# Kernel tuning notes

Hardware: AMD Instinct MI355X
Metric: run time of the kernel (lower is better)

## Reference

```python
import jax, jax.numpy as jnp
import numpy as np

N_NODES = 50000
N_EDGES = 800000
E_DIM = 128
N_LAYERS = 3
IN_DIM = 2
OUT_DIM = 1


def _lin_init(key, fan_in, fan_out, scale=None):
    # rough kaiming-tanh init, exact values don't matter for correctness testing
    s = scale if scale is not None else (5.0 / 3.0) / np.sqrt(fan_in)
    return jax.random.normal(key, (fan_in, fan_out), dtype=jnp.float32) * s


def setup_inputs() -> dict:
    key = jax.random.key(0)
    ks = jax.random.split(key, 16)
    node_feature = jax.random.normal(ks[0], (N_NODES, IN_DIM), dtype=jnp.float32)
    edge_index = jax.random.randint(ks[1], (2, N_EDGES), 0, N_NODES)
    batch = jnp.zeros((N_NODES,), dtype=jnp.int32)

    enc_W = _lin_init(ks[2], IN_DIM, E_DIM)
    enc_b = jnp.zeros((E_DIM,), dtype=jnp.float32)

    def stack(k, fan_in, fan_out):
        kk = jax.random.split(k, N_LAYERS)
        return jnp.stack([_lin_init(kk[i], fan_in, fan_out) for i in range(N_LAYERS)])

    gate_W = stack(ks[3], E_DIM, E_DIM)
    gate_b = jnp.zeros((N_LAYERS, E_DIM), dtype=jnp.float32)
    att_W = stack(ks[4], E_DIM, E_DIM)
    att_b = jnp.zeros((N_LAYERS, E_DIM), dtype=jnp.float32)
    msg_W = stack(ks[5], E_DIM, E_DIM)
    msg_b = jnp.zeros((N_LAYERS, E_DIM), dtype=jnp.float32)
    upd_W = stack(ks[6], 2 * E_DIM, E_DIM)
    upd_b = jnp.zeros((N_LAYERS, E_DIM), dtype=jnp.float32)

    dec1_W = _lin_init(ks[7], E_DIM, E_DIM // 2)
    dec1_b = jnp.zeros((E_DIM // 2,), dtype=jnp.float32)
    dec2_W = _lin_init(ks[8], E_DIM // 2, OUT_DIM, scale=1.0 / np.sqrt(E_DIM // 2))
    dec2_b = jnp.zeros((OUT_DIM,), dtype=jnp.float32)

    return dict(node_feature=node_feature, edge_index=edge_index, batch=batch,
                enc_W=enc_W, enc_b=enc_b,
                gate_W=gate_W, gate_b=gate_b, att_W=att_W, att_b=att_b,
                msg_W=msg_W, msg_b=msg_b, upd_W=upd_W, upd_b=upd_b,
                dec1_W=dec1_W, dec1_b=dec1_b, dec2_W=dec2_W, dec2_b=dec2_b)


def _segment_softmax(x, seg, num_segments):
    # PyG softmax over segments, numerically stable, per-channel
    m = jax.ops.segment_max(x, seg, num_segments=num_segments)
    m = jnp.where(jnp.isfinite(m), m, 0.0)
    e = jnp.exp(x - m[seg])
    s = jax.ops.segment_sum(e, seg, num_segments=num_segments)
    return e / (s[seg] + 1e-16)


def reference(node_feature, edge_index, batch,
              enc_W, enc_b, gate_W, gate_b, att_W, att_b,
              msg_W, msg_b, upd_W, upd_b,
              dec1_W, dec1_b, dec2_W, dec2_b):
    n = node_feature.shape[0]
    src, dst = edge_index[0], edge_index[1]  # j -> i (source_to_target)
    h = jnp.tanh(node_feature @ enc_W + enc_b)  # [N, E_DIM]
    for l in range(N_LAYERS):
        mj = jnp.tanh(h[src] @ msg_W[l] + msg_b[l])          # messages [Edges, E_DIM]
        gate = mj @ gate_W[l] + gate_b[l]                     # gate_nn (Linear only)
        alpha = _segment_softmax(gate, dst, n)                # softmax over incoming edges
        v = jnp.tanh(mj @ att_W[l] + att_b[l])                # attention_mlp
        aggr = jax.ops.segment_sum(alpha * v, dst, num_segments=n)
        h = jnp.tanh(jnp.concatenate([h, aggr], axis=1) @ upd_W[l] + upd_b[l])
    out = jnp.tanh(h @ dec1_W + dec1_b)
    out = out @ dec2_W + dec2_b
    return out
```

## Files before the change

### kernel.cpp

```cpp
#include <hip/hip_runtime.h>
#include <math.h>

#define ED 128
#define PROW 256

typedef _Float16 f16;
typedef _Float16 half8 __attribute__((ext_vector_type(8)));
typedef _Float16 half4 __attribute__((ext_vector_type(4)));
typedef float f32x4 __attribute__((ext_vector_type(4)));

static __device__ __forceinline__ float tanh_fast(float x) {
  float ax = fabsf(x);
  float e = __expf(2.0f * ax);
  float t = 1.0f - 2.0f / (e + 1.0f);
  return __builtin_copysignf(t, x);
}

template <int NT, int NBYTES>
static __device__ __forceinline__ void stage256(
    const char* __restrict__ gsrc, char* lds, int tid) {
  #pragma unroll
  for (int i = 0; i < NBYTES / (NT * 16); ++i) {
    int b = (i * NT + tid) * 16;
    int row = b >> 8;
    int sw = (b & 255) ^ ((row & 7) << 4);
    float4 v = *reinterpret_cast<const float4*>(gsrc + (size_t)row * 256 + sw);
    *reinterpret_cast<float4*>(lds + b) = v;
  }
}

static __device__ __forceinline__ half8 read_w(const char* Wsb, int col, int koff) {
  int byte = col * 256 + (koff ^ ((col & 7) << 4));
  return *reinterpret_cast<const half8*>(Wsb + byte);
}

template <int NT>
static __device__ __forceinline__ void stage512(
    const char* __restrict__ gsrc, char* lds, int tid) {
  #pragma unroll
  for (int i = 0; i < 32768 / (NT * 16); ++i) {
    int b = (i * NT + tid) * 16;
    int row = b >> 9;
    int sw = (b & 511) ^ ((row & 7) << 4);
    float4 v = *reinterpret_cast<const float4*>(gsrc + (size_t)row * 512 + sw);
    *reinterpret_cast<float4*>(lds + b) = v;
  }
}

static __device__ __forceinline__ half8 read_w512(const char* Wsb, int colL, int koff) {
  int byte = colL * 512 + (koff ^ ((colL & 7) << 4));
  return *reinterpret_cast<const half8*>(Wsb + byte);
}

__global__ __launch_bounds__(256) void encoder_kernel(
    const float* __restrict__ x, const float* __restrict__ W,
    const float* __restrict__ b, f16* __restrict__ h, int n) {
  int idx = blockIdx.x * blockDim.x + threadIdx.x;
  if (idx >= n * ED) return;
  int i = idx >> 7, c = idx & 127;
  float v = x[i * 2 + 0] * W[c] + x[i * 2 + 1] * W[ED + c] + b[c];
  h[idx] = (f16)tanh_fast(v);
}

__global__ __launch_bounds__(256) void transpose_w_kernel(
    const float* __restrict__ src, f16* __restrict__ dst, int K, int C, int total) {
  int idx = blockIdx.x * 256 + threadIdx.x;
  if (idx >= total) return;
  int kc = K * C;
  int m = idx / kc;
  int rem = idx - m * kc;
  int c = rem / K;
  int k = rem - c * K;
  dst[idx] = (f16)src[(size_t)m * kc + (size_t)k * C + c];
}

__global__ __launch_bounds__(256) void transpose3_kernel(
    const float* __restrict__ s0, const float* __restrict__ s1,
    const float* __restrict__ s2, f16* __restrict__ d0,
    f16* __restrict__ d1, f16* __restrict__ d2) {
  int idx = blockIdx.x * 256 + threadIdx.x;
  const int per = 3 * 128 * 128;
  int which = idx / per;
  if (which >= 3) return;
  int rem = idx - which * per;
  const float* s = (which == 0) ? s0 : (which == 1) ? s1 : s2;
  f16* d = (which == 0) ? d0 : (which == 1) ? d1 : d2;
  int m = rem >> 14;
  int r2 = rem & 16383;
  int c = r2 >> 7, k = r2 & 127;
  d[rem] = (f16)s[m * 16384 + k * 128 + c];
}

__global__ __launch_bounds__(256) void count_deg_kernel(
    const int* __restrict__ dst, int* __restrict__ deg, int E) {
  int e = blockIdx.x * blockDim.x + threadIdx.x;
  if (e < E) atomicAdd(&deg[dst[e]], 1);
}

__global__ __launch_bounds__(1024) void scan_kernel(
    const int* __restrict__ deg, int* __restrict__ offs,
    int* __restrict__ cursor, int n) {
  __shared__ int wsum[16];
  __shared__ int carry_s;
  const int tid = threadIdx.x;
  const int lane = tid & 63;
  const int wid = tid >> 6;
  if (tid == 0) carry_s = 0;
  __syncthreads();
  for (int base = 0; base < n; base += 1024) {
    const int i = base + tid;
    const int v = (i < n) ? deg[i] : 0;
    int x = v;
    #pragma unroll
    for (int d = 1; d < 64; d <<= 1) {
      int t = __shfl_up(x, d, 64);
      if (lane >= d) x += t;
    }
    if (lane == 63) wsum[wid] = x;
    __syncthreads();
    int wbase = 0, total = 0;
    #pragma unroll
    for (int w = 0; w < 16; ++w) {
      int s = wsum[w];
      if (w < wid) wbase += s;
      total += s;
    }
    const int carry = carry_s;
    if (i < n) {
      const int excl = carry + wbase + x - v;
      offs[i] = excl;
      cursor[i] = excl;
    }
    __syncthreads();
    if (tid == 0) carry_s = carry + total;
    __syncthreads();
  }
  if (tid == 0) offs[n] = carry_s;
}

__global__ __launch_bounds__(256) void scatter_kernel(
    const int* __restrict__ src, const int* __restrict__ dst,
    int* __restrict__ cursor, int* __restrict__ ssrc, int E) {
  int e = blockIdx.x * blockDim.x + threadIdx.x;
  if (e < E) {
    int d = dst[e];
    int pos = atomicAdd(&cursor[d], 1);
    ssrc[pos] = src[e];
  }
}


__global__ __launch_bounds__(512, 4) void gemm_mgv_kernel(
    const f16* __restrict__ h,
    const f16* __restrict__ mWt, const float* __restrict__ mb,
    const f16* __restrict__ gWt, const float* __restrict__ gb,
    const f16* __restrict__ aWt, const float* __restrict__ ab,
    f16* __restrict__ P, int n) {
  __shared__ f16 Ws[128 * 128];
  __shared__ f16 Ss[128 * 128];
  char* Wsb = reinterpret_cast<char*>(Ws);
  char* Sb = reinterpret_cast<char*>(Ss);
  const int tid = threadIdx.x;
  const int w = tid >> 6, lane = tid & 63;
  const int lr = lane & 15, lg = lane >> 4;
  const int r0 = blockIdx.x * 128 + w * 16;

  half8 a[4];
  {
    int rr = r0 + lr;
    if (rr >= n) rr = n - 1;
    const f16* ap = h + (size_t)rr * ED + lg * 8;
    #pragma unroll
    for (int kt = 0; kt < 4; ++kt)
      a[kt] = *reinterpret_cast<const half8*>(ap + kt * 32);
  }

  stage256<512, 32768>((const char*)mWt, Wsb, tid);
  __syncthreads();
  #pragma unroll
  for (int t = 0; t < 8; ++t) {
    f32x4 acc = {0.f, 0.f, 0.f, 0.f};
    int col = t * 16 + lr;
    #pragma unroll
    for (int kt = 0; kt < 4; ++kt)
      acc = __builtin_amdgcn_mfma_f32_16x16x32_f16(a[kt], read_w(Wsb, col, lg * 16 + kt * 64), acc, 0, 0, 0);
    float bias = mb[col];
    #pragma unroll
    for (int j = 0; j < 4; ++j) {
      int srow = w * 16 + lg * 4 + j;
      int byte = srow * 256 + (((col * 2) ^ ((srow & 7) << 4)));
      *reinterpret_cast<f16*>(Sb + byte) = (f16)tanh_fast(acc[j] + bias);
    }
  }
  half8 ma[4];
  {
    int lrow = w * 16 + lr;
    #pragma unroll
    for (int kt = 0; kt < 4; ++kt) {
      int byte = lrow * 256 + ((lg * 16 + kt * 64) ^ ((lrow & 7) << 4));
      ma[kt] = *reinterpret_cast<const half8*>(Sb + byte);
    }
  }
  __syncthreads();

  stage256<512, 32768>((const char*)gWt, Wsb, tid);
  __syncthreads();
  #pragma unroll
  for (int t = 0; t < 8; ++t) {
    f32x4 acc = {0.f, 0.f, 0.f, 0.f};
    int col = t * 16 + lr;
    #pragma unroll
    for (int kt = 0; kt < 4; ++kt)
      acc = __builtin_amdgcn_mfma_f32_16x16x32_f16(ma[kt], read_w(Wsb, col, lg * 16 + kt * 64), acc, 0, 0, 0);
    float bias = gb[col];
    #pragma unroll
    for (int j = 0; j < 4; ++j) {
      int grow = r0 + lg * 4 + j;
      if (grow < n)
        P[(size_t)grow * PROW + col] = (f16)fminf(__expf(acc[j] + bias), 60000.f);
    }
  }
  __syncthreads();

  stage256<512, 32768>((const char*)aWt, Wsb, tid);
  __syncthreads();
  #pragma unroll
  for (int t = 0; t < 8; ++t) {
    f32x4 acc = {0.f, 0.f, 0.f, 0.f};
    int col = t * 16 + lr;
    #pragma unroll
    for (int kt = 0; kt < 4; ++kt)
      acc = __builtin_amdgcn_mfma_f32_16x16x32_f16(ma[kt], read_w(Wsb, col, lg * 16 + kt * 64), acc, 0, 0, 0);
    float bias = ab[col];
    #pragma unroll
    for (int j = 0; j < 4; ++j) {
      int grow = r0 + lg * 4 + j;
      if (grow < n) {
        float wld = (float)P[(size_t)grow * PROW + col];
        P[(size_t)grow * PROW + 128 + col] = (f16)(wld * tanh_fast(acc[j] + bias));
      }
    }
  }
}

__global__ __launch_bounds__(512, 4) void updmgv_kernel(
    const f16* __restrict__ h, const f16* __restrict__ ag,
    const f16* __restrict__ uWt, const float* __restrict__ ub,
    const f16* __restrict__ mWt, const float* __restrict__ mb,
    const f16* __restrict__ gWt, const float* __restrict__ gb,
    const f16* __restrict__ aWt, const float* __restrict__ ab,
    f16* __restrict__ hout, f16* __restrict__ P, int n) {
  __shared__ f16 Ws[128 * 128];
  __shared__ f16 Ss[128 * 128];
  char* Wsb = reinterpret_cast<char*>(Ws);
  char* Sb = reinterpret_cast<char*>(Ss);
  const int tid = threadIdx.x;
  const int w = tid >> 6, lane = tid & 63;
  const int lr = lane & 15, lg = lane >> 4;
  const int r0 = blockIdx.x * 128 + w * 16;

  half8 ah[4], aa[4];
  {
    int rr = r0 + lr;
    if (rr >= n) rr = n - 1;
    const f16* ap = h + (size_t)rr * ED + lg * 8;
    const f16* bp = ag + (size_t)rr * ED + lg * 8;
    #pragma unroll
    for (int kt = 0; kt < 4; ++kt) {
      ah[kt] = *reinterpret_cast<const half8*>(ap + kt * 32);
      aa[kt] = *reinterpret_cast<const half8*>(bp + kt * 32);
    }
  }

  #pragma unroll
  for (int half = 0; half < 2; ++half) {
    __syncthreads();
    stage512<512>((const char*)uWt + (size_t)half * 64 * 512, Wsb, tid);
    __syncthreads();
    #pragma unroll
    for (int t = 0; t < 4; ++t) {
      int colL = t * 16 + lr;
      int col = half * 64 + colL;
      f32x4 acc = {0.f, 0.f, 0.f, 0.f};
      #pragma unroll
      for (int kt = 0; kt < 4; ++kt)
        acc = __builtin_amdgcn_mfma_f32_16x16x32_f16(ah[kt], read_w512(Wsb, colL, lg * 16 + kt * 64), acc, 0, 0, 0);
      #pragma unroll
      for (int kt = 0; kt < 4; ++kt)
        acc = __builtin_amdgcn_mfma_f32_16x16x32_f16(aa[kt], read_w512(Wsb, colL, 256 + lg * 16 + kt * 64), acc, 0, 0, 0);
      float bias = ub[col];
      #pragma unroll
      for (int j = 0; j < 4; ++j) {
        f16 hv = (f16)tanh_fast(acc[j] + bias);
        int srow = w * 16 + lg * 4 + j;
        int byte = srow * 256 + (((col * 2) ^ ((srow & 7) << 4)));
        *reinterpret_cast<f16*>(Sb + byte) = hv;
        int grow = r0 + lg * 4 + j;
        if (grow < n) hout[(size_t)grow * ED + col] = hv;
      }
    }
  }
  half8 ha[4];
  {
    int lrow = w * 16 + lr;
    #pragma unroll
    for (int kt = 0; kt < 4; ++kt) {
      int byte = lrow * 256 + ((lg * 16 + kt * 64) ^ ((lrow & 7) << 4));
      ha[kt] = *reinterpret_cast<const half8*>(Sb + byte);
    }
  }
  __syncthreads();

  stage256<512, 32768>((const char*)mWt, Wsb, tid);
  __syncthreads();
  #pragma unroll
  for (int t = 0; t < 8; ++t) {
    f32x4 acc = {0.f, 0.f, 0.f, 0.f};
    int col = t * 16 + lr;
    #pragma unroll
    for (int kt = 0; kt < 4; ++kt)
      acc = __builtin_amdgcn_mfma_f32_16x16x32_f16(ha[kt], read_w(Wsb, col, lg * 16 + kt * 64), acc, 0, 0, 0);
    float bias = mb[col];
    #pragma unroll
    for (int j = 0; j < 4; ++j) {
      int srow = w * 16 + lg * 4 + j;
      int byte = srow * 256 + (((col * 2) ^ ((srow & 7) << 4)));
      *reinterpret_cast<f16*>(Sb + byte) = (f16)tanh_fast(acc[j] + bias);
    }
  }
  half8 ma[4];
  {
    int lrow = w * 16 + lr;
    #pragma unroll
    for (int kt = 0; kt < 4; ++kt) {
      int byte = lrow * 256 + ((lg * 16 + kt * 64) ^ ((lrow & 7) << 4));
      ma[kt] = *reinterpret_cast<const half8*>(Sb + byte);
    }
  }
  __syncthreads();

  stage256<512, 32768>((const char*)gWt, Wsb, tid);
  __syncthreads();
  #pragma unroll
  for (int t = 0; t < 8; ++t) {
    f32x4 acc = {0.f, 0.f, 0.f, 0.f};
    int col = t * 16 + lr;
    #pragma unroll
    for (int kt = 0; kt < 4; ++kt)
      acc = __builtin_amdgcn_mfma_f32_16x16x32_f16(ma[kt], read_w(Wsb, col, lg * 16 + kt * 64), acc, 0, 0, 0);
    float bias = gb[col];
    #pragma unroll
    for (int j = 0; j < 4; ++j) {
      int grow = r0 + lg * 4 + j;
      if (grow < n)
        P[(size_t)grow * PROW + col] = (f16)fminf(__expf(acc[j] + bias), 60000.f);
    }
  }
  __syncthreads();

  stage256<512, 32768>((const char*)aWt, Wsb, tid);
  __syncthreads();
  #pragma unroll
  for (int t = 0; t < 8; ++t) {
    f32x4 acc = {0.f, 0.f, 0.f, 0.f};
    int col = t * 16 + lr;
    #pragma unroll
    for (int kt = 0; kt < 4; ++kt)
      acc = __builtin_amdgcn_mfma_f32_16x16x32_f16(ma[kt], read_w(Wsb, col, lg * 16 + kt * 64), acc, 0, 0, 0);
    float bias = ab[col];
    #pragma unroll
    for (int j = 0; j < 4; ++j) {
      int grow = r0 + lg * 4 + j;
      if (grow < n) {
        float wld = (float)P[(size_t)grow * PROW + col];
        P[(size_t)grow * PROW + 128 + col] = (f16)(wld * tanh_fast(acc[j] + bias));
      }
    }
  }
}

__global__ __launch_bounds__(512, 4) void upddec_kernel(
    const f16* __restrict__ h, const f16* __restrict__ ag,
    const f16* __restrict__ uWt, const float* __restrict__ ub,
    const f16* __restrict__ d1Wt, const float* __restrict__ d1b,
    const float* __restrict__ d2W, const float* __restrict__ d2b,
    float* __restrict__ out, int n) {
  __shared__ f16 Ws[128 * 128];
  __shared__ f16 Ss[128 * 128];
  char* Wsb = reinterpret_cast<char*>(Ws);
  char* Sb = reinterpret_cast<char*>(Ss);
  const int tid = threadIdx.x;
  const int w = tid >> 6, lane = tid & 63;
  const int lr = lane & 15, lg = lane >> 4;
  const int r0 = blockIdx.x * 128 + w * 16;

  half8 ah[4], aa[4];
  {
    int rr = r0 + lr;
    if (rr >= n) rr = n - 1;
    const f16* ap = h + (size_t)rr * ED + lg * 8;
    const f16* bp = ag + (size_t)rr * ED + lg * 8;
    #pragma unroll
    for (int kt = 0; kt < 4; ++kt) {
      ah[kt] = *reinterpret_cast<const half8*>(ap + kt * 32);
      aa[kt] = *reinterpret_cast<const half8*>(bp + kt * 32);
    }
  }

  #pragma unroll
  for (int half = 0; half < 2; ++half) {
    __syncthreads();
    stage512<512>((const char*)uWt + (size_t)half * 64 * 512, Wsb, tid);
    __syncthreads();
    #pragma unroll
    for (int t = 0; t < 4; ++t) {
      int colL = t * 16 + lr;
      int col = half * 64 + colL;
      f32x4 acc = {0.f, 0.f, 0.f, 0.f};
      #pragma unroll
      for (int kt = 0; kt < 4; ++kt)
        acc = __builtin_amdgcn_mfma_f32_16x16x32_f16(ah[kt], read_w512(Wsb, colL, lg * 16 + kt * 64), acc, 0, 0, 0);
      #pragma unroll
      for (int kt = 0; kt < 4; ++kt)
        acc = __builtin_amdgcn_mfma_f32_16x16x32_f16(aa[kt], read_w512(Wsb, colL, 256 + lg * 16 + kt * 64), acc, 0, 0, 0);
      float bias = ub[col];
      #pragma unroll
      for (int j = 0; j < 4; ++j) {
        int srow = w * 16 + lg * 4 + j;
        int byte = srow * 256 + (((col * 2) ^ ((srow & 7) << 4)));
        *reinterpret_cast<f16*>(Sb + byte) = (f16)tanh_fast(acc[j] + bias);
      }
    }
  }
  half8 ha[4];
  {
    int lrow = w * 16 + lr;
    #pragma unroll
    for (int kt = 0; kt < 4; ++kt) {
      int byte = lrow * 256 + ((lg * 16 + kt * 64) ^ ((lrow & 7) << 4));
      ha[kt] = *reinterpret_cast<const half8*>(Sb + byte);
    }
  }
  __syncthreads();

  stage256<512, 16384>((const char*)d1Wt, Wsb, tid);
  __syncthreads();
  float rowsum[4] = {0.f, 0.f, 0.f, 0.f};
  #pragma unroll
  for (int t = 0; t < 4; ++t) {
    f32x4 acc = {0.f, 0.f, 0.f, 0.f};
    int col = t * 16 + lr;
    #pragma unroll
    for (int kt = 0; kt < 4; ++kt)
      acc = __builtin_amdgcn_mfma_f32_16x16x32_f16(ha[kt], read_w(Wsb, col, lg * 16 + kt * 64), acc, 0, 0, 0);
    float b1 = d1b[col], w2 = d2W[col];
    #pragma unroll
    for (int j = 0; j < 4; ++j) rowsum[j] += tanh_fast(acc[j] + b1) * w2;
  }
  #pragma unroll
  for (int d = 1; d < 16; d <<= 1) {
    #pragma unroll
    for (int j = 0; j < 4; ++j) rowsum[j] += __shfl_xor(rowsum[j], d, 64);
  }
  if (lr == 0) {
    #pragma unroll
    for (int j = 0; j < 4; ++j) {
      int grow = r0 + lg * 4 + j;
      if (grow < n) out[grow] = rowsum[j] + d2b[0];
    }
  }
}

__global__ __launch_bounds__(256) void edge_aggr_kernel(
    const int* __restrict__ offs, const int* __restrict__ ssrc,
    const f16* __restrict__ P, f16* __restrict__ aggr, int n) {
  int i = blockIdx.x * 4 + (threadIdx.x >> 6);
  if (i >= n) return;
  int lane = threadIdx.x & 63;
  int s0 = offs[i], s1 = offs[i + 1];
  const char* Pb = reinterpret_cast<const char*>(P);

  float4 acc = {0.f, 0.f, 0.f, 0.f};
  #pragma unroll 4
  for (int e = s0; e < s1; ++e) {
    int sn = ssrc[e];
    half4 x = *reinterpret_cast<const half4*>(Pb + (size_t)sn * 512 + lane * 8);
    acc.x += (float)x.x;
    acc.y += (float)x.y;
    acc.z += (float)x.z;
    acc.w += (float)x.w;
  }
  float px = __shfl(acc.x, lane ^ 32, 64);
  float py = __shfl(acc.y, lane ^ 32, 64);
  float pz = __shfl(acc.z, lane ^ 32, 64);
  float pw = __shfl(acc.w, lane ^ 32, 64);
  if (lane >= 32) {
    half4 o;
    o.x = (f16)(acc.x / (px + 1e-16f));
    o.y = (f16)(acc.y / (py + 1e-16f));
    o.z = (f16)(acc.z / (pz + 1e-16f));
    o.w = (f16)(acc.w / (pw + 1e-16f));
    *reinterpret_cast<half4*>(
        reinterpret_cast<char*>(aggr) + (size_t)i * 256 + (size_t)(lane - 32) * 8) = o;
  }
}

extern "C" void kernel_launch(void* const* d_in, const int* in_sizes, int n_in,
                              void* d_out, int out_size, void* d_ws, size_t ws_size,
                              hipStream_t stream) {
  const float* node_feature = (const float*)d_in[0];
  const int*   edge_index   = (const int*)d_in[1];
  const float* enc_W  = (const float*)d_in[3];
  const float* enc_b  = (const float*)d_in[4];
  const float* gate_W = (const float*)d_in[5];
  const float* gate_b = (const float*)d_in[6];
  const float* att_W  = (const float*)d_in[7];
  const float* att_b  = (const float*)d_in[8];
  const float* msg_W  = (const float*)d_in[9];
  const float* msg_b  = (const float*)d_in[10];
  const float* upd_W  = (const float*)d_in[11];
  const float* upd_b  = (const float*)d_in[12];
  const float* dec1_W = (const float*)d_in[13];
  const float* dec1_b = (const float*)d_in[14];
  const float* dec2_W = (const float*)d_in[15];
  const float* dec2_b = (const float*)d_in[16];

  const int n = in_sizes[0] / 2;
  const int E = in_sizes[1] / 2;
  const int* src = edge_index;
  const int* dst = edge_index + E;

  char* ws = (char*)d_ws;
  size_t off = 0;
  auto alloc = [&](size_t bytes) -> void* {
    void* p = ws + off;
    off += (bytes + 255) & ~(size_t)255;
    return p;
  };
  f16* hA   = (f16*)alloc((size_t)n * ED * 2);
  f16* hB   = (f16*)alloc((size_t)n * ED * 2);
  f16* P    = (f16*)alloc((size_t)n * PROW * 2);
  f16* aggr = (f16*)alloc((size_t)n * ED * 2);
  int* deg    = (int*)alloc((size_t)n * 4);
  int* offs   = (int*)alloc((size_t)(n + 1) * 4);
  int* cursor = (int*)alloc((size_t)n * 4);
  int* ssrc   = (int*)alloc((size_t)E * 4);
  f16* msgT  = (f16*)alloc((size_t)3 * ED * ED * 2);
  f16* gateT = (f16*)alloc((size_t)3 * ED * ED * 2);
  f16* attT  = (f16*)alloc((size_t)3 * ED * ED * 2);
  f16* updT  = (f16*)alloc((size_t)3 * ED * 2 * ED * 2);
  f16* dec1T = (f16*)alloc((size_t)ED * 64 * 2);

  {
    int tot3 = 3 * 3 * ED * ED;
    transpose3_kernel<<<(tot3 + 255) / 256, 256, 0, stream>>>(
        msg_W, gate_W, att_W, msgT, gateT, attT);
    int totu = 3 * 2 * ED * ED;
    transpose_w_kernel<<<(totu + 255) / 256, 256, 0, stream>>>(
        upd_W, updT, 2 * ED, ED, totu);
    int totd = ED * 64;
    transpose_w_kernel<<<(totd + 255) / 256, 256, 0, stream>>>(
        dec1_W, dec1T, ED, 64, totd);
  }

  hipMemsetAsync(deg, 0, (size_t)n * 4, stream);
  count_deg_kernel<<<(E + 255) / 256, 256, 0, stream>>>(dst, deg, E);
  scan_kernel<<<1, 1024, 0, stream>>>(deg, offs, cursor, n);
  scatter_kernel<<<(E + 255) / 256, 256, 0, stream>>>(src, dst, cursor, ssrc, E);

  encoder_kernel<<<((size_t)n * ED + 255) / 256, 256, 0, stream>>>(
      node_feature, enc_W, enc_b, hA, n);

  const int gemm_grid = (n + 127) / 128;
  const int aggr_grid = (n + 3) / 4;

  gemm_mgv_kernel<<<gemm_grid, 512, 0, stream>>>(
      hA, msgT, msg_b, gateT, gate_b, attT, att_b, P, n);
  edge_aggr_kernel<<<aggr_grid, 256, 0, stream>>>(offs, ssrc, P, aggr, n);

  updmgv_kernel<<<gemm_grid, 512, 0, stream>>>(
      hA, aggr, updT, upd_b,
      msgT + (size_t)1 * ED * ED, msg_b + ED,
      gateT + (size_t)1 * ED * ED, gate_b + ED,
      attT + (size_t)1 * ED * ED, att_b + ED,
      hB, P, n);
  edge_aggr_kernel<<<aggr_grid, 256, 0, stream>>>(offs, ssrc, P, aggr, n);

  updmgv_kernel<<<gemm_grid, 512, 0, stream>>>(
      hB, aggr, updT + (size_t)1 * 2 * ED * ED, upd_b + ED,
      msgT + (size_t)2 * ED * ED, msg_b + 2 * ED,
      gateT + (size_t)2 * ED * ED, gate_b + 2 * ED,
      attT + (size_t)2 * ED * ED, att_b + 2 * ED,
      hA, P, n);
  edge_aggr_kernel<<<aggr_grid, 256, 0, stream>>>(offs, ssrc, P, aggr, n);

  upddec_kernel<<<gemm_grid, 512, 0, stream>>>(
      hA, aggr, updT + (size_t)2 * 2 * ED * ED, upd_b + 2 * ED,
      dec1T, dec1_b, dec2_W, dec2_b, (float*)d_out, n);
}
```

Baseline: 447.9 us.

## Prefetch weight panels into registers and interleave P layout to drop readback

Weight staging into LDS is split into a register load and an LDS write, so the next panel's global load is issued before the current GEMM and its latency overlaps compute. The gate and attention GEMMs are reordered: attention tanh values are held in registers, then the gate exp is computed and both (weight, weight*value) are written as interleaved half2 pairs. This removes the global read-back of P and the cross-lane shuffle and divide split in edge aggregation. The cost is extra register pressure from the prefetched panels and the tq array, which under the launch bounds could cause spills.

```diff
diff --git a/kernel.cpp b/kernel.cpp
--- a/kernel.cpp
+++ b/kernel.cpp
@@ -7,6 +7,7 @@
 typedef _Float16 f16;
 typedef _Float16 half8 __attribute__((ext_vector_type(8)));
 typedef _Float16 half4 __attribute__((ext_vector_type(4)));
+typedef _Float16 half2v __attribute__((ext_vector_type(2)));
 typedef float f32x4 __attribute__((ext_vector_type(4)));
 
 static __device__ __forceinline__ float tanh_fast(float x) {
@@ -16,37 +17,35 @@
   return __builtin_copysignf(t, x);
 }
 
-template <int NT, int NBYTES>
-static __device__ __forceinline__ void stage256(
-    const char* __restrict__ gsrc, char* lds, int tid) {
-  #pragma unroll
-  for (int i = 0; i < NBYTES / (NT * 16); ++i) {
+template <int NI>
+struct Panel { float4 v[NI]; };
+
+template <int NI, int NT, int RB>
+static __device__ __forceinline__ Panel<NI> panel_load(
+    const char* __restrict__ g, int tid) {
+  Panel<NI> p;
+  #pragma unroll
+  for (int i = 0; i < NI; ++i) {
     int b = (i * NT + tid) * 16;
-    int row = b >> 8;
-    int sw = (b & 255) ^ ((row & 7) << 4);
-    float4 v = *reinterpret_cast<const float4*>(gsrc + (size_t)row * 256 + sw);
-    *reinterpret_cast<float4*>(lds + b) = v;
-  }
+    int row = b / RB;
+    int sw = (b % RB) ^ ((row & 7) << 4);
+    p.v[i] = *reinterpret_cast<const float4*>(g + (size_t)row * RB + sw);
+  }
+  return p;
+}
+
+template <int NI, int NT>
+static __device__ __forceinline__ void panel_write(
+    char* lds, const Panel<NI>& p, int tid) {
+  #pragma unroll
+  for (int i = 0; i < NI; ++i)
+    *reinterpret_cast<float4*>(lds + (size_t)(i * NT + tid) * 16) = p.v[i];
 }
 
 static __device__ __forceinline__ half8 read_w(const char* Wsb, int col, int koff) {
   int byte = col * 256 + (koff ^ ((col & 7) << 4));
   return *reinterpret_cast<const half8*>(Wsb + byte);
 }
-
-template <int NT>
-static __device__ __forceinline__ void stage512(
-    const char* __restrict__ gsrc, char* lds, int tid) {
-  #pragma unroll
-  for (int i = 0; i < 32768 / (NT * 16); ++i) {
-    int b = (i * NT + tid) * 16;
-    int row = b >> 9;
-    int sw = (b & 511) ^ ((row & 7) << 4);
-    float4 v = *reinterpret_cast<const float4*>(gsrc + (size_t)row * 512 + sw);
-    *reinterpret_cast<float4*>(lds + b) = v;
-  }
-}
-
 static __device__ __forceinline__ half8 read_w512(const char* Wsb, int colL, int koff) {
   int byte = colL * 512 + (koff ^ ((colL & 7) << 4));
   return *reinterpret_cast<const half8*>(Wsb + byte);
@@ -161,10 +160,11 @@
   char* Wsb = reinterpret_cast<char*>(Ws);
   char* Sb = reinterpret_cast<char*>(Ss);
   const int tid = threadIdx.x;
-  const int w = tid >> 6, lane = tid & 63;
+  const int wd = tid >> 6, lane = tid & 63;
   const int lr = lane & 15, lg = lane >> 4;
-  const int r0 = blockIdx.x * 128 + w * 16;
-
+  const int r0 = blockIdx.x * 128 + wd * 16;
+
+  Panel<4> nx = panel_load<4, 512, 256>((const char*)mWt, tid);
   half8 a[4];
   {
     int rr = r0 + lr;
@@ -174,9 +174,10 @@
     for (int kt = 0; kt < 4; ++kt)
       a[kt] = *reinterpret_cast<const half8*>(ap + kt * 32);
   }
-
-  stage256<512, 32768>((const char*)mWt, Wsb, tid);
-  __syncthreads();
+  panel_write<4, 512>(Wsb, nx, tid);
+  nx = panel_load<4, 512, 256>((const char*)aWt, tid);
+  __syncthreads();
+
   #pragma unroll
   for (int t = 0; t < 8; ++t) {
     f32x4 acc = {0.f, 0.f, 0.f, 0.f};
@@ -187,14 +188,14 @@
     float bias = mb[col];
     #pragma unroll
     for (int j = 0; j < 4; ++j) {
-      int srow = w * 16 + lg * 4 + j;
+      int srow = wd * 16 + lg * 4 + j;
       int byte = srow * 256 + (((col * 2) ^ ((srow & 7) << 4)));
       *reinterpret_cast<f16*>(Sb + byte) = (f16)tanh_fast(acc[j] + bias);
     }
   }
   half8 ma[4];
   {
-    int lrow = w * 16 + lr;
+    int lrow = wd * 16 + lr;
     #pragma unroll
     for (int kt = 0; kt < 4; ++kt) {
       int byte = lrow * 256 + ((lg * 16 + kt * 64) ^ ((lrow & 7) << 4));
@@ -202,9 +203,26 @@
     }
   }
   __syncthreads();
-
-  stage256<512, 32768>((const char*)gWt, Wsb, tid);
-  __syncthreads();
+  panel_write<4, 512>(Wsb, nx, tid);
+  nx = panel_load<4, 512, 256>((const char*)gWt, tid);
+  __syncthreads();
+
+  half4 tq[8];
+  #pragma unroll
+  for (int t = 0; t < 8; ++t) {
+    f32x4 acc = {0.f, 0.f, 0.f, 0.f};
+    int col = t * 16 + lr;
+    #pragma unroll
+    for (int kt = 0; kt < 4; ++kt)
+      acc = __builtin_amdgcn_mfma_f32_16x16x32_f16(ma[kt], read_w(Wsb, col, lg * 16 + kt * 64), acc, 0, 0, 0);
+    float bias = ab[col];
+    #pragma unroll
+    for (int j = 0; j < 4; ++j) tq[t][j] = (f16)tanh_fast(acc[j] + bias);
+  }
+  __syncthreads();
+  panel_write<4, 512>(Wsb, nx, tid);
+  __syncthreads();
+
   #pragma unroll
   for (int t = 0; t < 8; ++t) {
     f32x4 acc = {0.f, 0.f, 0.f, 0.f};
@@ -216,28 +234,12 @@
     #pragma unroll
     for (int j = 0; j < 4; ++j) {
       int grow = r0 + lg * 4 + j;
-      if (grow < n)
-        P[(size_t)grow * PROW + col] = (f16)fminf(__expf(acc[j] + bias), 60000.f);
-    }
-  }
-  __syncthreads();
-
-  stage256<512, 32768>((const char*)aWt, Wsb, tid);
-  __syncthreads();
-  #pragma unroll
-  for (int t = 0; t < 8; ++t) {
-    f32x4 acc = {0.f, 0.f, 0.f, 0.f};
-    int col = t * 16 + lr;
-    #pragma unroll
-    for (int kt = 0; kt < 4; ++kt)
-      acc = __builtin_amdgcn_mfma_f32_16x16x32_f16(ma[kt], read_w(Wsb, col, lg * 16 + kt * 64), acc, 0, 0, 0);
-    float bias = ab[col];
-    #pragma unroll
-    for (int j = 0; j < 4; ++j) {
-      int grow = r0 + lg * 4 + j;
       if (grow < n) {
-        float wld = (float)P[(size_t)grow * PROW + col];
-        P[(size_t)grow * PROW + 128 + col] = (f16)(wld * tanh_fast(acc[j] + bias));
+        float wexp = fminf(__expf(acc[j] + bias), 60000.f);
+        half2v pr;
+        pr.x = (f16)wexp;
+        pr.y = (f16)(wexp * (float)tq[t][j]);
+        *reinterpret_cast<half2v*>(P + (size_t)grow * PROW + col * 2) = pr;
       }
     }
   }
@@ -255,10 +257,11 @@
   char* Wsb = reinterpret_cast<char*>(Ws);
   char* Sb = reinterpret_cast<char*>(Ss);
   const int tid = threadIdx.x;
-  const int w = tid >> 6, lane = tid & 63;
+  const int wd = tid >> 6, lane = tid & 63;
   const int lr = lane & 15, lg = lane >> 4;
-  const int r0 = blockIdx.x * 128 + w * 16;
-
+  const int r0 = blockIdx.x * 128 + wd * 16;
+
+  Panel<4> nx = panel_load<4, 512, 512>((const char*)uWt, tid);
   half8 ah[4], aa[4];
   {
     int rr = r0 + lr;
@@ -271,38 +274,62 @@
       aa[kt] = *reinterpret_cast<const half8*>(bp + kt * 32);
     }
   }
-
-  #pragma unroll
-  for (int half = 0; half < 2; ++half) {
-    __syncthreads();
-    stage512<512>((const char*)uWt + (size_t)half * 64 * 512, Wsb, tid);
-    __syncthreads();
-    #pragma unroll
-    for (int t = 0; t < 4; ++t) {
-      int colL = t * 16 + lr;
-      int col = half * 64 + colL;
-      f32x4 acc = {0.f, 0.f, 0.f, 0.f};
-      #pragma unroll
-      for (int kt = 0; kt < 4; ++kt)
-        acc = __builtin_amdgcn_mfma_f32_16x16x32_f16(ah[kt], read_w512(Wsb, colL, lg * 16 + kt * 64), acc, 0, 0, 0);
-      #pragma unroll
-      for (int kt = 0; kt < 4; ++kt)
-        acc = __builtin_amdgcn_mfma_f32_16x16x32_f16(aa[kt], read_w512(Wsb, colL, 256 + lg * 16 + kt * 64), acc, 0, 0, 0);
-      float bias = ub[col];
-      #pragma unroll
-      for (int j = 0; j < 4; ++j) {
-        f16 hv = (f16)tanh_fast(acc[j] + bias);
-        int srow = w * 16 + lg * 4 + j;
-        int byte = srow * 256 + (((col * 2) ^ ((srow & 7) << 4)));
-        *reinterpret_cast<f16*>(Sb + byte) = hv;
-        int grow = r0 + lg * 4 + j;
-        if (grow < n) hout[(size_t)grow * ED + col] = hv;
-      }
+  panel_write<4, 512>(Wsb, nx, tid);
+  nx = panel_load<4, 512, 512>((const char*)uWt + 64 * 512, tid);
+  __syncthreads();
+
+  #pragma unroll
+  for (int t = 0; t < 4; ++t) {
+    int colL = t * 16 + lr;
+    int col = colL;
+    f32x4 acc = {0.f, 0.f, 0.f, 0.f};
+    #pragma unroll
+    for (int kt = 0; kt < 4; ++kt)
+      acc = __builtin_amdgcn_mfma_f32_16x16x32_f16(ah[kt], read_w512(Wsb, colL, lg * 16 + kt * 64), acc, 0, 0, 0);
+    #pragma unroll
+    for (int kt = 0; kt < 4; ++kt)
+      acc = __builtin_amdgcn_mfma_f32_16x16x32_f16(aa[kt], read_w512(Wsb, colL, 256 + lg * 16 + kt * 64), acc, 0, 0, 0);
+    float bias = ub[col];
+    #pragma unroll
+    for (int j = 0; j < 4; ++j) {
+      f16 hv = (f16)tanh_fast(acc[j] + bias);
+      int srow = wd * 16 + lg * 4 + j;
+      int byte = srow * 256 + (((col * 2) ^ ((srow & 7) << 4)));
+      *reinterpret_cast<f16*>(Sb + byte) = hv;
+      int grow = r0 + lg * 4 + j;
+      if (grow < n) hout[(size_t)grow * ED + col] = hv;
+    }
+  }
+  __syncthreads();
+  panel_write<4, 512>(Wsb, nx, tid);
+  nx = panel_load<4, 512, 256>((const char*)mWt, tid);
+  __syncthreads();
+
+  #pragma unroll
+  for (int t = 0; t < 4; ++t) {
+    int colL = t * 16 + lr;
+    int col = 64 + colL;
+    f32x4 acc = {0.f, 0.f, 0.f, 0.f};
+    #pragma unroll
+    for (int kt = 0; kt < 4; ++kt)
+      acc = __builtin_amdgcn_mfma_f32_16x16x32_f16(ah[kt], read_w512(Wsb, colL, lg * 16 + kt * 64), acc, 0, 0, 0);
+    #pragma unroll
+    for (int kt = 0; kt < 4; ++kt)
+      acc = __builtin_amdgcn_mfma_f32_16x16x32_f16(aa[kt], read_w512(Wsb, colL, 256 + lg * 16 + kt * 64), acc, 0, 0, 0);
+    float bias = ub[col];
+    #pragma unroll
+    for (int j = 0; j < 4; ++j) {
+      f16 hv = (f16)tanh_fast(acc[j] + bias);
+      int srow = wd * 16 + lg * 4 + j;
+      int byte = srow * 256 + (((col * 2) ^ ((srow & 7) << 4)));
+      *reinterpret_cast<f16*>(Sb + byte) = hv;
+      int grow = r0 + lg * 4 + j;
+      if (grow < n) hout[(size_t)grow * ED + col] = hv;
     }
   }
   half8 ha[4];
   {
-    int lrow = w * 16 + lr;
+    int lrow = wd * 16 + lr;
     #pragma unroll
     for (int kt = 0; kt < 4; ++kt) {
       int byte = lrow * 256 + ((lg * 16 + kt * 64) ^ ((lrow & 7) << 4));
@@ -310,9 +337,10 @@
     }
   }
   __syncthreads();
-
-  stage256<512, 32768>((const char*)mWt, Wsb, tid);
-  __syncthreads();
+  panel_write<4, 512>(Wsb, nx, tid);
+  nx = panel_load<4, 512, 256>((const char*)aWt, tid);
+  __syncthreads();
+
   #pragma unroll
   for (int t = 0; t < 8; ++t) {
     f32x4 acc = {0.f, 0.f, 0.f, 0.f};
@@ -323,14 +351,14 @@
     float bias = mb[col];
     #pragma unroll
     for (int j = 0; j < 4; ++j) {
-      int srow = w * 16 + lg * 4 + j;
+      int srow = wd * 16 + lg * 4 + j;
       int byte = srow * 256 + (((col * 2) ^ ((srow & 7) << 4)));
       *reinterpret_cast<f16*>(Sb + byte) = (f16)tanh_fast(acc[j] + bias);
     }
   }
   half8 ma[4];
   {
-    int lrow = w * 16 + lr;
+    int lrow = wd * 16 + lr;
     #pragma unroll
     for (int kt = 0; kt < 4; ++kt) {
       int byte = lrow * 256 + ((lg * 16 + kt * 64) ^ ((lrow & 7) << 4));
@@ -338,9 +366,26 @@
     }
   }
   __syncthreads();
-
-  stage256<512, 32768>((const char*)gWt, Wsb, tid);
-  __syncthreads();
+  panel_write<4, 512>(Wsb, nx, tid);
+  nx = panel_load<4, 512, 256>((const char*)gWt, tid);
+  __syncthreads();
+
+  half4 tq[8];
+  #pragma unroll
+  for (int t = 0; t < 8; ++t) {
+    f32x4 acc = {0.f, 0.f, 0.f, 0.f};
+    int col = t * 16 + lr;
+    #pragma unroll
+    for (int kt = 0; kt < 4; ++kt)
+      acc = __builtin_amdgcn_mfma_f32_16x16x32_f16(ma[kt], read_w(Wsb, col, lg * 16 + kt * 64), acc, 0, 0, 0);
+    float bias = ab[col];
+    #pragma unroll
+    for (int j = 0; j < 4; ++j) tq[t][j] = (f16)tanh_fast(acc[j] + bias);
+  }
+  __syncthreads();
+  panel_write<4, 512>(Wsb, nx, tid);
+  __syncthreads();
+
   #pragma unroll
   for (int t = 0; t < 8; ++t) {
     f32x4 acc = {0.f, 0.f, 0.f, 0.f};
@@ -352,28 +397,12 @@
     #pragma unroll
     for (int j = 0; j < 4; ++j) {
       int grow = r0 + lg * 4 + j;
-      if (grow < n)
-        P[(size_t)grow * PROW + col] = (f16)fminf(__expf(acc[j] + bias), 60000.f);
-    }
-  }
-  __syncthreads();
-
-  stage256<512, 32768>((const char*)aWt, Wsb, tid);
-  __syncthreads();
-  #pragma unroll
-  for (int t = 0; t < 8; ++t) {
-    f32x4 acc = {0.f, 0.f, 0.f, 0.f};
-    int col = t * 16 + lr;
-    #pragma unroll
-    for (int kt = 0; kt < 4; ++kt)
-      acc = __builtin_amdgcn_mfma_f32_16x16x32_f16(ma[kt], read_w(Wsb, col, lg * 16 + kt * 64), acc, 0, 0, 0);
-    float bias = ab[col];
-    #pragma unroll
-    for (int j = 0; j < 4; ++j) {
-      int grow = r0 + lg * 4 + j;
       if (grow < n) {
-        float wld = (float)P[(size_t)grow * PROW + col];
-        P[(size_t)grow * PROW + 128 + col] = (f16)(wld * tanh_fast(acc[j] + bias));
+        float wexp = fminf(__expf(acc[j] + bias), 60000.f);
+        half2v pr;
+        pr.x = (f16)wexp;
+        pr.y = (f16)(wexp * (float)tq[t][j]);
+        *reinterpret_cast<half2v*>(P + (size_t)grow * PROW + col * 2) = pr;
       }
     }
   }
@@ -390,10 +419,11 @@
   char* Wsb = reinterpret_cast<char*>(Ws);
   char* Sb = reinterpret_cast<char*>(Ss);
   const int tid = threadIdx.x;
-  const int w = tid >> 6, lane = tid & 63;
+  const int wd = tid >> 6, lane = tid & 63;
   const int lr = lane & 15, lg = lane >> 4;
-  const int r0 = blockIdx.x * 128 + w * 16;
-
+  const int r0 = blockIdx.x * 128 + wd * 16;
+
+  Panel<4> nx = panel_load<4, 512, 512>((const char*)uWt, tid);
   half8 ah[4], aa[4];
   {
     int rr = r0 + lr;
@@ -406,35 +436,56 @@
       aa[kt] = *reinterpret_cast<const half8*>(bp + kt * 32);
     }
   }
-
-  #pragma unroll
-  for (int half = 0; half < 2; ++half) {
-    __syncthreads();
-    stage512<512>((const char*)uWt + (size_t)half * 64 * 512, Wsb, tid);
-    __syncthreads();
-    #pragma unroll
-    for (int t = 0; t < 4; ++t) {
-      int colL = t * 16 + lr;
-      int col = half * 64 + colL;
-      f32x4 acc = {0.f, 0.f, 0.f, 0.f};
-      #pragma unroll
-      for (int kt = 0; kt < 4; ++kt)
-        acc = __builtin_amdgcn_mfma_f32_16x16x32_f16(ah[kt], read_w512(Wsb, colL, lg * 16 + kt * 64), acc, 0, 0, 0);
-      #pragma unroll
-      for (int kt = 0; kt < 4; ++kt)
-        acc = __builtin_amdgcn_mfma_f32_16x16x32_f16(aa[kt], read_w512(Wsb, colL, 256 + lg * 16 + kt * 64), acc, 0, 0, 0);
-      float bias = ub[col];
-      #pragma unroll
-      for (int j = 0; j < 4; ++j) {
-        int srow = w * 16 + lg * 4 + j;
-        int byte = srow * 256 + (((col * 2) ^ ((srow & 7) << 4)));
-        *reinterpret_cast<f16*>(Sb + byte) = (f16)tanh_fast(acc[j] + bias);
-      }
+  panel_write<4, 512>(Wsb, nx, tid);
+  nx = panel_load<4, 512, 512>((const char*)uWt + 64 * 512, tid);
+  __syncthreads();
+
+  #pragma unroll
+  for (int t = 0; t < 4; ++t) {
+    int colL = t * 16 + lr;
+    int col = colL;
+    f32x4 acc = {0.f, 0.f, 0.f, 0.f};
+    #pragma unroll
+    for (int kt = 0; kt < 4; ++kt)
+      acc = __builtin_amdgcn_mfma_f32_16x16x32_f16(ah[kt], read_w512(Wsb, colL, lg * 16 + kt * 64), acc, 0, 0, 0);
+    #pragma unroll
+    for (int kt = 0; kt < 4; ++kt)
+      acc = __builtin_amdgcn_mfma_f32_16x16x32_f16(aa[kt], read_w512(Wsb, colL, 256 + lg * 16 + kt * 64), acc, 0, 0, 0);
+    float bias = ub[col];
+    #pragma unroll
+    for (int j = 0; j < 4; ++j) {
+      int srow = wd * 16 + lg * 4 + j;
+      int byte = srow * 256 + (((col * 2) ^ ((srow & 7) << 4)));
+      *reinterpret_cast<f16*>(Sb + byte) = (f16)tanh_fast(acc[j] + bias);
+    }
+  }
+  __syncthreads();
+  panel_write<4, 512>(Wsb, nx, tid);
+  Panel<2> nd = panel_load<2, 512, 256>((const char*)d1Wt, tid);
+  __syncthreads();
+
+  #pragma unroll
+  for (int t = 0; t < 4; ++t) {
+    int colL = t * 16 + lr;
+    int col = 64 + colL;
+    f32x4 acc = {0.f, 0.f, 0.f, 0.f};
+    #pragma unroll
+    for (int kt = 0; kt < 4; ++kt)
+      acc = __builtin_amdgcn_mfma_f32_16x16x32_f16(ah[kt], read_w512(Wsb, colL, lg * 16 + kt * 64), acc, 0, 0, 0);
+    #pragma unroll
+    for (int kt = 0; kt < 4; ++kt)
+      acc = __builtin_amdgcn_mfma_f32_16x16x32_f16(aa[kt], read_w512(Wsb, colL, 256 + lg * 16 + kt * 64), acc, 0, 0, 0);
+    float bias = ub[col];
+    #pragma unroll
+    for (int j = 0; j < 4; ++j) {
+      int srow = wd * 16 + lg * 4 + j;
+      int byte = srow * 256 + (((col * 2) ^ ((srow & 7) << 4)));
+      *reinterpret_cast<f16*>(Sb + byte) = (f16)tanh_fast(acc[j] + bias);
     }
   }
   half8 ha[4];
   {
-    int lrow = w * 16 + lr;
+    int lrow = wd * 16 + lr;
     #pragma unroll
     for (int kt = 0; kt < 4; ++kt) {
       int byte = lrow * 256 + ((lg * 16 + kt * 64) ^ ((lrow & 7) << 4));
@@ -442,9 +493,9 @@
     }
   }
   __syncthreads();
-
-  stage256<512, 16384>((const char*)d1Wt, Wsb, tid);
-  __syncthreads();
+  panel_write<2, 512>(Wsb, nd, tid);
+  __syncthreads();
+
   float rowsum[4] = {0.f, 0.f, 0.f, 0.f};
   #pragma unroll
   for (int t = 0; t < 4; ++t) {
@@ -480,29 +531,21 @@
   int s0 = offs[i], s1 = offs[i + 1];
   const char* Pb = reinterpret_cast<const char*>(P);
 
-  float4 acc = {0.f, 0.f, 0.f, 0.f};
+  float sw0 = 0.f, wv0 = 0.f, sw1 = 0.f, wv1 = 0.f;
   #pragma unroll 4
   for (int e = s0; e < s1; ++e) {
     int sn = ssrc[e];
     half4 x = *reinterpret_cast<const half4*>(Pb + (size_t)sn * 512 + lane * 8);
-    acc.x += (float)x.x;
-    acc.y += (float)x.y;
-    acc.z += (float)x.z;
-    acc.w += (float)x.w;
-  }
-  float px = __shfl(acc.x, lane ^ 32, 64);
-  float py = __shfl(acc.y, lane ^ 32, 64);
-  float pz = __shfl(acc.z, lane ^ 32, 64);
-  float pw = __shfl(acc.w, lane ^ 32, 64);
-  if (lane >= 32) {
-    half4 o;
-    o.x = (f16)(acc.x / (px + 1e-16f));
-    o.y = (f16)(acc.y / (py + 1e-16f));
-    o.z = (f16)(acc.z / (pz + 1e-16f));
-    o.w = (f16)(acc.w / (pw + 1e-16f));
-    *reinterpret_cast<half4*>(
-        reinterpret_cast<char*>(aggr) + (size_t)i * 256 + (size_t)(lane - 32) * 8) = o;
-  }
+    sw0 += (float)x.x;
+    wv0 += (float)x.y;
+    sw1 += (float)x.z;
+    wv1 += (float)x.w;
+  }
+  half2v o;
+  o.x = (f16)(wv0 / (sw0 + 1e-16f));
+  o.y = (f16)(wv1 / (sw1 + 1e-16f));
+  *reinterpret_cast<half2v*>(
+      reinterpret_cast<char*>(aggr) + (size_t)i * 256 + (size_t)lane * 4) = o;
 }
 
 extern "C" void kernel_launch(void* const* d_in, const int* in_sizes, int n_in,
```

New measurement: 450.2 us. About the same (+0.5%).
